# Performance work log

Hardware: AMD Instinct MI355X
Metric: run time of the kernel (lower is better)

Reference implementation:

```python
import jax, jax.numpy as jnp
import numpy as np

N = 20000
IN_C = 512
HID = 64
H1 = 8
OUT_C = 256
E = 320000
NEG_SLOPE = 0.2


def gat_conv(x, src, dst, W, a_src, a_dst, b, concat):
    # PyG GATConv (shared lin for src/dst), inference mode (no dropout).
    H, C = a_src.shape
    h = (x @ W).reshape(N, H, C)                      # [N,H,C]
    alpha_src = (h * a_src[None]).sum(-1)             # [N,H]
    alpha_dst = (h * a_dst[None]).sum(-1)             # [N,H]
    alpha = jax.nn.leaky_relu(alpha_src[src] + alpha_dst[dst], NEG_SLOPE)  # [E,H]
    # segment softmax over incoming edges of each dst node
    amax = jax.ops.segment_max(alpha, dst, num_segments=N)
    amax = jnp.where(jnp.isfinite(amax), amax, 0.0)
    ex = jnp.exp(alpha - amax[dst])
    denom = jax.ops.segment_sum(ex, dst, num_segments=N)
    coef = ex / (denom[dst] + 1e-16)                  # [E,H]
    msg = h[src] * coef[:, :, None]                   # [E,H,C]
    out = jax.ops.segment_sum(msg, dst, num_segments=N)  # [N,H,C]
    out = out.reshape(N, H * C) if concat else out.mean(axis=1)
    return out + b


def setup_inputs() -> dict:
    key = jax.random.key(0)
    ks = jax.random.split(key, 10)
    x = jax.random.normal(ks[0], (N, IN_C), dtype=jnp.float32)
    edge_index = jax.random.randint(ks[1], (2, E), 0, N, dtype=jnp.int32)
    s1 = 1.0 / np.sqrt(IN_C)
    s2 = 1.0 / np.sqrt(HID * H1)
    W1 = jax.random.uniform(ks[2], (IN_C, H1 * HID), jnp.float32, -s1, s1)
    att_src1 = jax.random.uniform(ks[3], (H1, HID), jnp.float32, -s1, s1)
    att_dst1 = jax.random.uniform(ks[4], (H1, HID), jnp.float32, -s1, s1)
    b1 = jnp.zeros((H1 * HID,), jnp.float32)
    W2 = jax.random.uniform(ks[5], (H1 * HID, OUT_C), jnp.float32, -s2, s2)
    att_src2 = jax.random.uniform(ks[6], (1, OUT_C), jnp.float32, -s2, s2)
    att_dst2 = jax.random.uniform(ks[7], (1, OUT_C), jnp.float32, -s2, s2)
    b2 = jnp.zeros((OUT_C,), jnp.float32)
    return {"x": x, "edge_index": edge_index, "W1": W1, "att_src1": att_src1,
            "att_dst1": att_dst1, "b1": b1, "W2": W2, "att_src2": att_src2,
            "att_dst2": att_dst2, "b2": b2}


def reference(x, edge_index, W1, att_src1, att_dst1, b1, W2, att_src2, att_dst2, b2):
    # add self-loops (PyG GATConv default add_self_loops=True)
    loop = jnp.arange(N, dtype=edge_index.dtype)
    src = jnp.concatenate([edge_index[0], loop])
    dst = jnp.concatenate([edge_index[1], loop])
    h = gat_conv(x, src, dst, W1, att_src1, att_dst1, b1, concat=True)
    h = jax.nn.elu(h)
    out = gat_conv(h, src, dst, W2, att_src2, att_dst2, b2, concat=False)
    return jax.nn.log_softmax(out, axis=1)
```

## Files before the change

### kernel.cpp

```cpp
#include <hip/hip_runtime.h>
#include <math.h>

#define N_NODES 20000
#define IN_CH   512
#define HID_TOT 512
#define OUT_CH  256
#define N_EDGE  320000
#define TOT_EDGE (N_EDGE + N_NODES)

typedef __attribute__((ext_vector_type(8))) short short8;
typedef __attribute__((ext_vector_type(4))) float f32x4;
typedef __attribute__((ext_vector_type(2))) float f32x2;

__device__ __forceinline__ ushort f2bf(float f) {
    union { float f; unsigned u; } v; v.f = f;
    unsigned u = v.u;
    return (ushort)((u + 0x7fffu + ((u >> 16) & 1u)) >> 16);
}

__device__ __forceinline__ void glds16(const ushort* g, ushort* l) {
    __builtin_amdgcn_global_load_lds(
        (const __attribute__((address_space(1))) void*)g,
        (__attribute__((address_space(3))) void*)l, 16, 0, 0);
}

__device__ __forceinline__ float lrelu(float a) { return fmaxf(a, 0.2f * a); }

#define NA_BLK (N_NODES * IN_CH / 4 / 256)
#define NB_BLK ((IN_CH / 64) * (HID_TOT / 4))
#define NC_BLK ((HID_TOT / 64) * (OUT_CH / 4))
#define NZ_BLK ((N_NODES + 255) / 256)
__global__ __launch_bounds__(256) void prep_kernel(const float* __restrict__ x,
                                                   ushort* __restrict__ xb,
                                                   const float* __restrict__ W1,
                                                   ushort* __restrict__ w1t,
                                                   const float* __restrict__ W2,
                                                   ushort* __restrict__ w2t,
                                                   int* __restrict__ counts,
                                                   float* __restrict__ as2,
                                                   float* __restrict__ ad2) {
    int b = blockIdx.x;
    int t = threadIdx.x;
    if (b < NA_BLK) {
        int i = b * 256 + t;
        float4 v = *(const float4*)&x[(size_t)i * 4];
        ushort4 o = make_ushort4(f2bf(v.x), f2bf(v.y), f2bf(v.z), f2bf(v.w));
        *(ushort4*)&xb[(size_t)i * 4] = o;
    } else if (b < NA_BLK + NB_BLK) {
        int bb = b - NA_BLK;
        int k = (bb & 7) * 64 + (t & 63);
        int n = (bb >> 3) * 4 + (t >> 6);
        w1t[(size_t)n * IN_CH + k] = f2bf(W1[(size_t)k * HID_TOT + n]);
    } else if (b < NA_BLK + NB_BLK + NC_BLK) {
        int bb = b - NA_BLK - NB_BLK;
        int k = (bb & 7) * 64 + (t & 63);
        int n = (bb >> 3) * 4 + (t >> 6);
        w2t[(size_t)n * HID_TOT + k] = f2bf(W2[(size_t)k * OUT_CH + n]);
    } else {
        int i = (b - NA_BLK - NB_BLK - NC_BLK) * 256 + t;
        if (i < N_NODES) { counts[i] = 0; as2[i] = 0.f; ad2[i] = 0.f; }
    }
}

__global__ void hist_kernel(const int* __restrict__ ei, int* __restrict__ counts) {
    int e = blockIdx.x * blockDim.x + threadIdx.x;
    if (e >= TOT_EDGE) return;
    int d = (e < N_EDGE) ? ei[N_EDGE + e] : (e - N_EDGE);
    atomicAdd(&counts[d], 1);
}

__global__ __launch_bounds__(1024) void scan_kernel(const int* __restrict__ counts,
                                                    int* __restrict__ offsets,
                                                    int* __restrict__ cursors) {
    const int C = (N_NODES + 1023) / 1024;
    int t = threadIdx.x;
    int lane = t & 63, wid = t >> 6;
    int base = t * C;
    int sum = 0;
#pragma unroll
    for (int i = 0; i < C; i++) {
        int idx = base + i;
        if (idx < N_NODES) sum += counts[idx];
    }
    int val = sum;
#pragma unroll
    for (int off = 1; off < 64; off <<= 1) {
        int y = __shfl_up(val, off);
        if (lane >= off) val += y;
    }
    __shared__ int wsum[16], woff[16], stotal;
    if (lane == 63) wsum[wid] = val;
    __syncthreads();
    if (t == 0) {
        int r = 0;
        for (int w = 0; w < 16; w++) { woff[w] = r; r += wsum[w]; }
        stotal = r;
    }
    __syncthreads();
    int running = woff[wid] + (val - sum);
#pragma unroll
    for (int i = 0; i < C; i++) {
        int idx = base + i;
        if (idx < N_NODES) {
            offsets[idx] = running;
            cursors[idx] = running;
            running += counts[idx];
        }
    }
    if (t == 0) offsets[N_NODES] = stotal;
}

__global__ void scatter_kernel(const int* __restrict__ ei, int* __restrict__ cursors,
                               int* __restrict__ srcs) {
    int e = blockIdx.x * blockDim.x + threadIdx.x;
    if (e >= TOT_EDGE) return;
    int s, d;
    if (e < N_EDGE) { s = ei[e]; d = ei[N_EDGE + e]; } else { s = e - N_EDGE; d = s; }
    int pos = atomicAdd(&cursors[d], 1);
    srcs[pos] = s;
}

__global__ __launch_bounds__(256, 2) void gemm_mfma_kernel(const ushort* __restrict__ A,
                                                           const ushort* __restrict__ Bt,
                                                           unsigned char* __restrict__ Cf8,
                                                           const float* __restrict__ asrc,
                                                           const float* __restrict__ adst,
                                                           float* __restrict__ as_out,
                                                           float* __restrict__ ad_out,
                                                           int M, int N, int K, int layer1) {
    __shared__ ushort As[128 * 64];
    __shared__ ushort Bs[128 * 64];
    int t = threadIdx.x;
    int lane = t & 63;
    int wave = t >> 6;
    int wr = (wave >> 1) * 64;
    int wc = (wave & 1) * 64;
    int bm = blockIdx.y * 128, bn = blockIdx.x * 128;
    int q = lane >> 4, l15 = lane & 15;

    const ushort* Aptr[4]; ushort* Alds[4];
    const ushort* Bptr[4]; ushort* Blds[4];
#pragma unroll
    for (int k = 0; k < 4; k++) {
        int c = t + 256 * k;
        int r = c >> 3, kqs = c & 7;
        int kqg = kqs ^ (r & 7);
        int ar = bm + r; if (ar >= M) ar = M - 1;
        Aptr[k] = A + (size_t)ar * K + kqg * 8;
        Alds[k] = &As[c * 8];
        Bptr[k] = Bt + (size_t)(bn + r) * K + kqg * 8;
        Blds[k] = &Bs[c * 8];
    }

    f32x4 acc[4][4];
#pragma unroll
    for (int i = 0; i < 4; i++)
#pragma unroll
        for (int j = 0; j < 4; j++) acc[i][j] = f32x4{0.f, 0.f, 0.f, 0.f};

    for (int k0 = 0; k0 < K; k0 += 64) {
        __syncthreads();
        glds16(Aptr[0] + k0, Alds[0]);
        glds16(Aptr[1] + k0, Alds[1]);
        glds16(Aptr[2] + k0, Alds[2]);
        glds16(Aptr[3] + k0, Alds[3]);
        glds16(Bptr[0] + k0, Blds[0]);
        glds16(Bptr[1] + k0, Blds[1]);
        glds16(Bptr[2] + k0, Blds[2]);
        glds16(Bptr[3] + k0, Blds[3]);
        __syncthreads();

#pragma unroll
        for (int s = 0; s < 2; s++) {
            int kq = s * 4 + q;
            short8 af[4], bf[4];
#pragma unroll
            for (int i = 0; i < 4; i++) {
                int row = wr + i * 16 + l15;
                int slot = kq ^ (row & 7);
                af[i] = *(const short8*)&As[row * 64 + slot * 8];
            }
#pragma unroll
            for (int j = 0; j < 4; j++) {
                int row = wc + j * 16 + l15;
                int slot = kq ^ (row & 7);
                bf[j] = *(const short8*)&Bs[row * 64 + slot * 8];
            }
#pragma unroll
            for (int i = 0; i < 4; i++)
#pragma unroll
                for (int j = 0; j < 4; j++)
                    acc[i][j] = __builtin_amdgcn_mfma_f32_16x16x32_bf16(af[i], bf[j], acc[i][j], 0, 0, 0);
        }
    }

    float av[4], dv[4];
#pragma unroll
    for (int j = 0; j < 4; j++) {
        int cg = bn + wc + j * 16 + l15;
        av[j] = asrc[cg];
        dv[j] = adst[cg];
    }
    float ps[4][4], pd[4][4];
#pragma unroll
    for (int i = 0; i < 4; i++)
#pragma unroll
        for (int r = 0; r < 4; r++) {
            float p = 0.f, d = 0.f;
#pragma unroll
            for (int j = 0; j < 4; j++) {
                p = fmaf(acc[i][j][r], av[j], p);
                d = fmaf(acc[i][j][r], dv[j], d);
            }
            ps[i][r] = p; pd[i][r] = d;
        }
#pragma unroll
    for (int off = 1; off < 16; off <<= 1) {
#pragma unroll
        for (int i = 0; i < 4; i++)
#pragma unroll
            for (int r = 0; r < 4; r++) {
                ps[i][r] += __shfl_xor(ps[i][r], off);
                pd[i][r] += __shfl_xor(pd[i][r], off);
            }
    }

    int hidx = blockIdx.x * 2 + (wave & 1);
#pragma unroll
    for (int i = 0; i < 4; i++) {
#pragma unroll
        for (int r = 0; r < 4; r++) {
            int rg = bm + wr + i * 16 + q * 4 + r;
            if (rg < M) {
#pragma unroll
                for (int j = 0; j < 4; j++) {
                    int cg = bn + wc + j * 16 + l15;
                    int w8 = __builtin_amdgcn_cvt_pk_fp8_f32(acc[i][j][r], acc[i][j][r], 0, false);
                    Cf8[(size_t)rg * N + cg] = (unsigned char)(w8 & 0xff);
                }
                if (l15 == 0) {
                    if (layer1) {
                        as_out[rg * 8 + hidx] = ps[i][r];
                        ad_out[rg * 8 + hidx] = pd[i][r];
                    } else {
                        atomicAdd(&as_out[rg], ps[i][r]);
                        atomicAdd(&ad_out[rg], pd[i][r]);
                    }
                }
            }
        }
    }
}

__global__ __launch_bounds__(256) void agg1_kernel(const unsigned char* __restrict__ h1f,
                                                   const float* __restrict__ as1,
                                                   const float* __restrict__ ad1,
                                                   const int* __restrict__ offsets,
                                                   const int* __restrict__ srcs,
                                                   const float* __restrict__ b1,
                                                   ushort* __restrict__ h1ab) {
    int v = blockIdx.x * 4 + (threadIdx.x >> 6);
    int lane = threadIdx.x & 63;
    int h = lane >> 3;
    int c8 = lane << 3;
    int s = offsets[v], e = offsets[v + 1];
    float adv = ad1[v * 8 + h];

    float denom = 0.f;
    float acc[8];
#pragma unroll
    for (int k = 0; k < 8; k++) acc[k] = 0.f;

    int i = s;
    for (; i + 8 <= e; i += 8) {
        int sn[8];
#pragma unroll
        for (int j = 0; j < 8; j++) sn[j] = srcs[i + j];
        uint2 r[8];
#pragma unroll
        for (int j = 0; j < 8; j++)
            r[j] = *(const uint2*)&h1f[(size_t)sn[j] * HID_TOT + c8];
        float w[8];
#pragma unroll
        for (int j = 0; j < 8; j++) {
            float a = lrelu(as1[sn[j] * 8 + h] + adv);
            w[j] = __expf(a);
            denom += w[j];
        }
#pragma unroll
        for (int j = 0; j < 8; j++) {
            f32x2 pa = __builtin_amdgcn_cvt_pk_f32_fp8(r[j].x, false);
            f32x2 pb = __builtin_amdgcn_cvt_pk_f32_fp8(r[j].x, true);
            f32x2 pc = __builtin_amdgcn_cvt_pk_f32_fp8(r[j].y, false);
            f32x2 pdd = __builtin_amdgcn_cvt_pk_f32_fp8(r[j].y, true);
            acc[0] = fmaf(w[j], pa.x, acc[0]); acc[1] = fmaf(w[j], pa.y, acc[1]);
            acc[2] = fmaf(w[j], pb.x, acc[2]); acc[3] = fmaf(w[j], pb.y, acc[3]);
            acc[4] = fmaf(w[j], pc.x, acc[4]); acc[5] = fmaf(w[j], pc.y, acc[5]);
            acc[6] = fmaf(w[j], pdd.x, acc[6]); acc[7] = fmaf(w[j], pdd.y, acc[7]);
        }
    }
    for (; i + 4 <= e; i += 4) {
        int sn[4];
#pragma unroll
        for (int j = 0; j < 4; j++) sn[j] = srcs[i + j];
        uint2 r[4];
#pragma unroll
        for (int j = 0; j < 4; j++)
            r[j] = *(const uint2*)&h1f[(size_t)sn[j] * HID_TOT + c8];
#pragma unroll
        for (int j = 0; j < 4; j++) {
            float a = lrelu(as1[sn[j] * 8 + h] + adv);
            float w = __expf(a);
            denom += w;
            f32x2 pa = __builtin_amdgcn_cvt_pk_f32_fp8(r[j].x, false);
            f32x2 pb = __builtin_amdgcn_cvt_pk_f32_fp8(r[j].x, true);
            f32x2 pc = __builtin_amdgcn_cvt_pk_f32_fp8(r[j].y, false);
            f32x2 pdd = __builtin_amdgcn_cvt_pk_f32_fp8(r[j].y, true);
            acc[0] = fmaf(w, pa.x, acc[0]); acc[1] = fmaf(w, pa.y, acc[1]);
            acc[2] = fmaf(w, pb.x, acc[2]); acc[3] = fmaf(w, pb.y, acc[3]);
            acc[4] = fmaf(w, pc.x, acc[4]); acc[5] = fmaf(w, pc.y, acc[5]);
            acc[6] = fmaf(w, pdd.x, acc[6]); acc[7] = fmaf(w, pdd.y, acc[7]);
        }
    }
    for (; i < e; i++) {
        int sn = srcs[i];
        uint2 r = *(const uint2*)&h1f[(size_t)sn * HID_TOT + c8];
        float a = lrelu(as1[sn * 8 + h] + adv);
        float w = __expf(a);
        denom += w;
        f32x2 pa = __builtin_amdgcn_cvt_pk_f32_fp8(r.x, false);
        f32x2 pb = __builtin_amdgcn_cvt_pk_f32_fp8(r.x, true);
        f32x2 pc = __builtin_amdgcn_cvt_pk_f32_fp8(r.y, false);
        f32x2 pdd = __builtin_amdgcn_cvt_pk_f32_fp8(r.y, true);
        acc[0] = fmaf(w, pa.x, acc[0]); acc[1] = fmaf(w, pa.y, acc[1]);
        acc[2] = fmaf(w, pb.x, acc[2]); acc[3] = fmaf(w, pb.y, acc[3]);
        acc[4] = fmaf(w, pc.x, acc[4]); acc[5] = fmaf(w, pc.y, acc[5]);
        acc[6] = fmaf(w, pdd.x, acc[6]); acc[7] = fmaf(w, pdd.y, acc[7]);
    }

    float inv = 1.f / (denom + 1e-16f);
    short8 ov;
#pragma unroll
    for (int k = 0; k < 8; k++) {
        float o = acc[k] * inv + b1[c8 + k];
        o = (o > 0.f) ? o : expm1f(o);
        ov[k] = (short)f2bf(o);
    }
    *(short8*)&h1ab[(size_t)v * HID_TOT + c8] = ov;
}

__global__ __launch_bounds__(256) void agg2_kernel(const unsigned char* __restrict__ h2f,
                                                   const float* __restrict__ as2,
                                                   const float* __restrict__ ad2,
                                                   const int* __restrict__ offsets,
                                                   const int* __restrict__ srcs,
                                                   const float* __restrict__ b2,
                                                   float* __restrict__ out) {
    int v = blockIdx.x * 4 + (threadIdx.x >> 6);
    int lane = threadIdx.x & 63;
    int c4 = lane << 2;
    int s = offsets[v], e = offsets[v + 1];
    float adv = ad2[v];

    float denom = 0.f;
    float acc[4];
#pragma unroll
    for (int k = 0; k < 4; k++) acc[k] = 0.f;

    int i = s;
    for (; i + 8 <= e; i += 8) {
        int sn[8];
#pragma unroll
        for (int j = 0; j < 8; j++) sn[j] = srcs[i + j];
        unsigned u[8];
#pragma unroll
        for (int j = 0; j < 8; j++)
            u[j] = *(const unsigned*)&h2f[(size_t)sn[j] * OUT_CH + c4];
        float w[8];
#pragma unroll
        for (int j = 0; j < 8; j++) {
            float a = lrelu(as2[sn[j]] + adv);
            w[j] = __expf(a);
            denom += w[j];
        }
#pragma unroll
        for (int j = 0; j < 8; j++) {
            f32x2 pa = __builtin_amdgcn_cvt_pk_f32_fp8(u[j], false);
            f32x2 pb = __builtin_amdgcn_cvt_pk_f32_fp8(u[j], true);
            acc[0] = fmaf(w[j], pa.x, acc[0]); acc[1] = fmaf(w[j], pa.y, acc[1]);
            acc[2] = fmaf(w[j], pb.x, acc[2]); acc[3] = fmaf(w[j], pb.y, acc[3]);
        }
    }
    for (; i + 4 <= e; i += 4) {
        int sn[4];
#pragma unroll
        for (int j = 0; j < 4; j++) sn[j] = srcs[i + j];
        unsigned u[4];
#pragma unroll
        for (int j = 0; j < 4; j++)
            u[j] = *(const unsigned*)&h2f[(size_t)sn[j] * OUT_CH + c4];
#pragma unroll
        for (int j = 0; j < 4; j++) {
            float a = lrelu(as2[sn[j]] + adv);
            float w = __expf(a);
            denom += w;
            f32x2 pa = __builtin_amdgcn_cvt_pk_f32_fp8(u[j], false);
            f32x2 pb = __builtin_amdgcn_cvt_pk_f32_fp8(u[j], true);
            acc[0] = fmaf(w, pa.x, acc[0]); acc[1] = fmaf(w, pa.y, acc[1]);
            acc[2] = fmaf(w, pb.x, acc[2]); acc[3] = fmaf(w, pb.y, acc[3]);
        }
    }
    for (; i < e; i++) {
        int sn = srcs[i];
        unsigned u = *(const unsigned*)&h2f[(size_t)sn * OUT_CH + c4];
        float a = lrelu(as2[sn] + adv);
        float w = __expf(a);
        denom += w;
        f32x2 pa = __builtin_amdgcn_cvt_pk_f32_fp8(u, false);
        f32x2 pb = __builtin_amdgcn_cvt_pk_f32_fp8(u, true);
        acc[0] = fmaf(w, pa.x, acc[0]); acc[1] = fmaf(w, pa.y, acc[1]);
        acc[2] = fmaf(w, pb.x, acc[2]); acc[3] = fmaf(w, pb.y, acc[3]);
    }

    float inv = 1.f / (denom + 1e-16f);
    float4 bb = *(const float4*)&b2[c4];
    float4 x;
    x.x = acc[0] * inv + bb.x; x.y = acc[1] * inv + bb.y;
    x.z = acc[2] * inv + bb.z; x.w = acc[3] * inv + bb.w;

    float mm = fmaxf(fmaxf(x.x, x.y), fmaxf(x.z, x.w));
#pragma unroll
    for (int off = 1; off < 64; off <<= 1) mm = fmaxf(mm, __shfl_xor(mm, off));
    float sum = __expf(x.x - mm) + __expf(x.y - mm) + __expf(x.z - mm) + __expf(x.w - mm);
#pragma unroll
    for (int off = 1; off < 64; off <<= 1) sum += __shfl_xor(sum, off);
    float ls = logf(sum);
    float4 o;
    o.x = x.x - mm - ls; o.y = x.y - mm - ls; o.z = x.z - mm - ls; o.w = x.w - mm - ls;
    *(float4*)&out[(size_t)v * OUT_CH + c4] = o;
}

static inline size_t align256(size_t x) { return (x + 255) & ~(size_t)255; }

extern "C" void kernel_launch(void* const* d_in, const int* in_sizes, int n_in,
                              void* d_out, int out_size, void* d_ws, size_t ws_size,
                              hipStream_t stream) {
    const float* x    = (const float*)d_in[0];
    const int*   ei   = (const int*)d_in[1];
    const float* W1   = (const float*)d_in[2];
    const float* as1w = (const float*)d_in[3];
    const float* ad1w = (const float*)d_in[4];
    const float* b1   = (const float*)d_in[5];
    const float* W2   = (const float*)d_in[6];
    const float* as2w = (const float*)d_in[7];
    const float* ad2w = (const float*)d_in[8];
    const float* b2   = (const float*)d_in[9];
    float* out = (float*)d_out;

    char* p = (char*)d_ws;
    unsigned char* h1f = (unsigned char*)p; p += align256((size_t)N_NODES * HID_TOT);
    unsigned char* h2f = (unsigned char*)p; p += align256((size_t)N_NODES * OUT_CH);
    ushort* xb   = (ushort*)p; p += align256(sizeof(ushort) * (size_t)N_NODES * IN_CH);
    ushort* h1ab = xb;
    ushort* w1t  = (ushort*)p; p += align256(sizeof(ushort) * (size_t)IN_CH * HID_TOT);
    ushort* w2t  = (ushort*)p; p += align256(sizeof(ushort) * (size_t)HID_TOT * OUT_CH);
    float* as1  = (float*)p; p += align256(sizeof(float) * (size_t)N_NODES * 8);
    float* ad1  = (float*)p; p += align256(sizeof(float) * (size_t)N_NODES * 8);
    float* as2  = (float*)p; p += align256(sizeof(float) * (size_t)N_NODES);
    float* ad2  = (float*)p; p += align256(sizeof(float) * (size_t)N_NODES);
    int* counts  = (int*)p; p += align256(sizeof(int) * (size_t)N_NODES);
    int* offsets = (int*)p; p += align256(sizeof(int) * (size_t)(N_NODES + 1));
    int* cursors = (int*)p; p += align256(sizeof(int) * (size_t)N_NODES);
    int* srcs    = (int*)p; p += align256(sizeof(int) * (size_t)TOT_EDGE);

    prep_kernel<<<NA_BLK + NB_BLK + NC_BLK + NZ_BLK, 256, 0, stream>>>(
        x, xb, W1, w1t, W2, w2t, counts, as2, ad2);

    int eb = (TOT_EDGE + 255) / 256;
    hist_kernel<<<eb, 256, 0, stream>>>(ei, counts);
    scan_kernel<<<1, 1024, 0, stream>>>(counts, offsets, cursors);
    scatter_kernel<<<eb, 256, 0, stream>>>(ei, cursors, srcs);

    gemm_mfma_kernel<<<dim3(HID_TOT / 128, (N_NODES + 127) / 128), 256, 0, stream>>>(
        xb, w1t, h1f, as1w, ad1w, as1, ad1, N_NODES, HID_TOT, IN_CH, 1);
    agg1_kernel<<<(N_NODES + 3) / 4, 256, 0, stream>>>(h1f, as1, ad1, offsets, srcs, b1, h1ab);

    gemm_mfma_kernel<<<dim3(OUT_CH / 128, (N_NODES + 127) / 128), 256, 0, stream>>>(
        h1ab, w2t, h2f, as2w, ad2w, as2, ad2, N_NODES, OUT_CH, HID_TOT, 0);
    agg2_kernel<<<(N_NODES + 3) / 4, 256, 0, stream>>>(h2f, as2, ad2, offsets, srcs, b2, out);
}
```

Baseline: 276.5 us.

## Split layer-1 aggregation per head and run layer-2 aggregation one wave per block

Layer-1 aggregation is remapped so each block handles a single attention head for 16 nodes. Sixteen lanes cover the head's 64 channels, four per lane, instead of one wave spanning all 512 channels of one node. The aim is to spread each node's gather over more independent waves and fewer registers, raising occupancy and latency hiding for the irregular neighbour reads. The cost is that each source row is fetched eight times in narrower 4-byte pieces, and the edge indices and source scores are read once per head. Layer-2 aggregation now launches 64-thread blocks, one node per block, instead of four nodes per 256-thread block.

New measurement: 275.6 us. No clear change (-0.3%).

```diff
diff --git a/kernel.cpp b/kernel.cpp
--- a/kernel.cpp
+++ b/kernel.cpp
@@ -259,106 +259,82 @@
                                                    const int* __restrict__ srcs,
                                                    const float* __restrict__ b1,
                                                    ushort* __restrict__ h1ab) {
-    int v = blockIdx.x * 4 + (threadIdx.x >> 6);
-    int lane = threadIdx.x & 63;
-    int h = lane >> 3;
-    int c8 = lane << 3;
+    int b = blockIdx.x;
+    int head = b & 7;
+    int grp = b >> 3;
+    int t = threadIdx.x;
+    int wave = t >> 6, lane = t & 63;
+    int qq = lane >> 4, l4 = lane & 15;
+    int v = grp * 16 + wave * 4 + qq;
+    int cofs = head * 64 + l4 * 4;
     int s = offsets[v], e = offsets[v + 1];
-    float adv = ad1[v * 8 + h];
+    float adv = ad1[v * 8 + head];
 
     float denom = 0.f;
-    float acc[8];
-#pragma unroll
-    for (int k = 0; k < 8; k++) acc[k] = 0.f;
+    float acc[4] = {0.f, 0.f, 0.f, 0.f};
 
     int i = s;
-    for (; i + 8 <= e; i += 8) {
-        int sn[8];
-#pragma unroll
-        for (int j = 0; j < 8; j++) sn[j] = srcs[i + j];
-        uint2 r[8];
-#pragma unroll
-        for (int j = 0; j < 8; j++)
-            r[j] = *(const uint2*)&h1f[(size_t)sn[j] * HID_TOT + c8];
-        float w[8];
-#pragma unroll
-        for (int j = 0; j < 8; j++) {
-            float a = lrelu(as1[sn[j] * 8 + h] + adv);
+    for (; i + 4 <= e; i += 4) {
+        int sn[4];
+#pragma unroll
+        for (int j = 0; j < 4; j++) sn[j] = srcs[i + j];
+        unsigned u[4];
+#pragma unroll
+        for (int j = 0; j < 4; j++)
+            u[j] = *(const unsigned*)&h1f[(size_t)sn[j] * HID_TOT + cofs];
+        float w[4];
+#pragma unroll
+        for (int j = 0; j < 4; j++) {
+            float a = lrelu(as1[sn[j] * 8 + head] + adv);
             w[j] = __expf(a);
             denom += w[j];
         }
 #pragma unroll
-        for (int j = 0; j < 8; j++) {
-            f32x2 pa = __builtin_amdgcn_cvt_pk_f32_fp8(r[j].x, false);
-            f32x2 pb = __builtin_amdgcn_cvt_pk_f32_fp8(r[j].x, true);
-            f32x2 pc = __builtin_amdgcn_cvt_pk_f32_fp8(r[j].y, false);
-            f32x2 pdd = __builtin_amdgcn_cvt_pk_f32_fp8(r[j].y, true);
+        for (int j = 0; j < 4; j++) {
+            f32x2 pa = __builtin_amdgcn_cvt_pk_f32_fp8(u[j], false);
+            f32x2 pb = __builtin_amdgcn_cvt_pk_f32_fp8(u[j], true);
             acc[0] = fmaf(w[j], pa.x, acc[0]); acc[1] = fmaf(w[j], pa.y, acc[1]);
             acc[2] = fmaf(w[j], pb.x, acc[2]); acc[3] = fmaf(w[j], pb.y, acc[3]);
-            acc[4] = fmaf(w[j], pc.x, acc[4]); acc[5] = fmaf(w[j], pc.y, acc[5]);
-            acc[6] = fmaf(w[j], pdd.x, acc[6]); acc[7] = fmaf(w[j], pdd.y, acc[7]);
-        }
-    }
-    for (; i + 4 <= e; i += 4) {
-        int sn[4];
-#pragma unroll
-        for (int j = 0; j < 4; j++) sn[j] = srcs[i + j];
-        uint2 r[4];
-#pragma unroll
-        for (int j = 0; j < 4; j++)
-            r[j] = *(const uint2*)&h1f[(size_t)sn[j] * HID_TOT + c8];
-#pragma unroll
-        for (int j = 0; j < 4; j++) {
-            float a = lrelu(as1[sn[j] * 8 + h] + adv);
-            float w = __expf(a);
-            denom += w;
-            f32x2 pa = __builtin_amdgcn_cvt_pk_f32_fp8(r[j].x, false);
-            f32x2 pb = __builtin_amdgcn_cvt_pk_f32_fp8(r[j].x, true);
-            f32x2 pc = __builtin_amdgcn_cvt_pk_f32_fp8(r[j].y, false);
-            f32x2 pdd = __builtin_amdgcn_cvt_pk_f32_fp8(r[j].y, true);
-            acc[0] = fmaf(w, pa.x, acc[0]); acc[1] = fmaf(w, pa.y, acc[1]);
-            acc[2] = fmaf(w, pb.x, acc[2]); acc[3] = fmaf(w, pb.y, acc[3]);
-            acc[4] = fmaf(w, pc.x, acc[4]); acc[5] = fmaf(w, pc.y, acc[5]);
-            acc[6] = fmaf(w, pdd.x, acc[6]); acc[7] = fmaf(w, pdd.y, acc[7]);
         }
     }
     for (; i < e; i++) {
         int sn = srcs[i];
-        uint2 r = *(const uint2*)&h1f[(size_t)sn * HID_TOT + c8];
-        float a = lrelu(as1[sn * 8 + h] + adv);
+        unsigned u = *(const unsigned*)&h1f[(size_t)sn * HID_TOT + cofs];
+        float a = lrelu(as1[sn * 8 + head] + adv);
         float w = __expf(a);
         denom += w;
-        f32x2 pa = __builtin_amdgcn_cvt_pk_f32_fp8(r.x, false);
-        f32x2 pb = __builtin_amdgcn_cvt_pk_f32_fp8(r.x, true);
-        f32x2 pc = __builtin_amdgcn_cvt_pk_f32_fp8(r.y, false);
-        f32x2 pdd = __builtin_amdgcn_cvt_pk_f32_fp8(r.y, true);
+        f32x2 pa = __builtin_amdgcn_cvt_pk_f32_fp8(u, false);
+        f32x2 pb = __builtin_amdgcn_cvt_pk_f32_fp8(u, true);
         acc[0] = fmaf(w, pa.x, acc[0]); acc[1] = fmaf(w, pa.y, acc[1]);
         acc[2] = fmaf(w, pb.x, acc[2]); acc[3] = fmaf(w, pb.y, acc[3]);
-        acc[4] = fmaf(w, pc.x, acc[4]); acc[5] = fmaf(w, pc.y, acc[5]);
-        acc[6] = fmaf(w, pdd.x, acc[6]); acc[7] = fmaf(w, pdd.y, acc[7]);
     }
 
     float inv = 1.f / (denom + 1e-16f);
-    short8 ov;
-#pragma unroll
-    for (int k = 0; k < 8; k++) {
-        float o = acc[k] * inv + b1[c8 + k];
-        o = (o > 0.f) ? o : expm1f(o);
-        ov[k] = (short)f2bf(o);
-    }
-    *(short8*)&h1ab[(size_t)v * HID_TOT + c8] = ov;
-}
-
-__global__ __launch_bounds__(256) void agg2_kernel(const unsigned char* __restrict__ h2f,
-                                                   const float* __restrict__ as2,
-                                                   const float* __restrict__ ad2,
-                                                   const int* __restrict__ offsets,
-                                                   const int* __restrict__ srcs,
-                                                   const float* __restrict__ b2,
-                                                   float* __restrict__ out) {
-    int v = blockIdx.x * 4 + (threadIdx.x >> 6);
-    int lane = threadIdx.x & 63;
-    int c4 = lane << 2;
+    ushort4 ov;
+    {
+        float o0 = acc[0] * inv + b1[cofs + 0];
+        float o1 = acc[1] * inv + b1[cofs + 1];
+        float o2 = acc[2] * inv + b1[cofs + 2];
+        float o3 = acc[3] * inv + b1[cofs + 3];
+        o0 = (o0 > 0.f) ? o0 : expm1f(o0);
+        o1 = (o1 > 0.f) ? o1 : expm1f(o1);
+        o2 = (o2 > 0.f) ? o2 : expm1f(o2);
+        o3 = (o3 > 0.f) ? o3 : expm1f(o3);
+        ov = make_ushort4(f2bf(o0), f2bf(o1), f2bf(o2), f2bf(o3));
+    }
+    *(ushort4*)&h1ab[(size_t)v * HID_TOT + cofs] = ov;
+}
+
+__global__ __launch_bounds__(64) void agg2_kernel(const unsigned char* __restrict__ h2f,
+                                                  const float* __restrict__ as2,
+                                                  const float* __restrict__ ad2,
+                                                  const int* __restrict__ offsets,
+                                                  const int* __restrict__ srcs,
+                                                  const float* __restrict__ b2,
+                                                  float* __restrict__ out) {
+    int v = blockIdx.x;
+    int t = threadIdx.x;
+    int c4 = t << 2;
     int s = offsets[v], e = offsets[v + 1];
     float adv = ad2[v];
 
@@ -483,9 +459,9 @@
 
     gemm_mfma_kernel<<<dim3(HID_TOT / 128, (N_NODES + 127) / 128), 256, 0, stream>>>(
         xb, w1t, h1f, as1w, ad1w, as1, ad1, N_NODES, HID_TOT, IN_CH, 1);
-    agg1_kernel<<<(N_NODES + 3) / 4, 256, 0, stream>>>(h1f, as1, ad1, offsets, srcs, b1, h1ab);
+    agg1_kernel<<<1250 * 8, 256, 0, stream>>>(h1f, as1, ad1, offsets, srcs, b1, h1ab);
 
     gemm_mfma_kernel<<<dim3(OUT_CH / 128, (N_NODES + 127) / 128), 256, 0, stream>>>(
         h1ab, w2t, h2f, as2w, ad2w, as2, ad2, N_NODES, OUT_CH, HID_TOT, 0);
-    agg2_kernel<<<(N_NODES + 3) / 4, 256, 0, stream>>>(h2f, as2, ad2, offsets, srcs, b2, out);
-}
+    agg2_kernel<<<N_NODES, 64, 0, stream>>>(h2f, as2, ad2, offsets, srcs, b2, out);
+}
```

## Remap aggregation kernels so each wave handles several nodes per head slice

Applied to the files above, without the earlier changes.

Layer-1 aggregation now gives each 64-lane block one head and 8 destination nodes, with 8 lanes per node reading 64 contiguous fp8 bytes. The attention-score arrays are stored head-major so those lanes read contiguous scores. Layer-2 aggregation handles two nodes per wave with 32 lanes each reading 8 bytes, and the log-softmax reduction shrinks to 32 lanes. The goal is to spread the gather latency of long edge lists across more independent nodes per wave. The trade-off is that different nodes in a wave have different degrees, causing divergence, and each source row of h1 is now fetched in eight separate head-sized pieces.

New measurement: 271.4 us. No clear change (-1.8%).

```diff
diff --git a/kernel.cpp b/kernel.cpp
--- a/kernel.cpp
+++ b/kernel.cpp
@@ -240,8 +240,8 @@
                 }
                 if (l15 == 0) {
                     if (layer1) {
-                        as_out[rg * 8 + hidx] = ps[i][r];
-                        ad_out[rg * 8 + hidx] = pd[i][r];
+                        as_out[hidx * N_NODES + rg] = ps[i][r];
+                        ad_out[hidx * N_NODES + rg] = pd[i][r];
                     } else {
                         atomicAdd(&as_out[rg], ps[i][r]);
                         atomicAdd(&ad_out[rg], pd[i][r]);
@@ -252,19 +252,25 @@
     }
 }
 
-__global__ __launch_bounds__(256) void agg1_kernel(const unsigned char* __restrict__ h1f,
-                                                   const float* __restrict__ as1,
-                                                   const float* __restrict__ ad1,
-                                                   const int* __restrict__ offsets,
-                                                   const int* __restrict__ srcs,
-                                                   const float* __restrict__ b1,
-                                                   ushort* __restrict__ h1ab) {
-    int v = blockIdx.x * 4 + (threadIdx.x >> 6);
-    int lane = threadIdx.x & 63;
-    int h = lane >> 3;
-    int c8 = lane << 3;
+__global__ __launch_bounds__(64) void agg1_kernel(const unsigned char* __restrict__ h1f,
+                                                  const float* __restrict__ as1,
+                                                  const float* __restrict__ ad1,
+                                                  const int* __restrict__ offsets,
+                                                  const int* __restrict__ srcs,
+                                                  const float* __restrict__ b1,
+                                                  ushort* __restrict__ h1ab) {
+    int b = blockIdx.x;
+    int head = b & 7;
+    int grp = b >> 3;
+    int lane = threadIdx.x;
+    int sub = lane >> 3;
+    int l8 = lane & 7;
+    int v = grp * 8 + sub;
+    int cofs = head * 64 + l8 * 8;
+    const unsigned char* hb = h1f + cofs;
+    const float* as1h = as1 + head * N_NODES;
     int s = offsets[v], e = offsets[v + 1];
-    float adv = ad1[v * 8 + h];
+    float adv = ad1[head * N_NODES + v];
 
     float denom = 0.f;
     float acc[8];
@@ -272,23 +278,23 @@
     for (int k = 0; k < 8; k++) acc[k] = 0.f;
 
     int i = s;
-    for (; i + 8 <= e; i += 8) {
-        int sn[8];
-#pragma unroll
-        for (int j = 0; j < 8; j++) sn[j] = srcs[i + j];
-        uint2 r[8];
-#pragma unroll
-        for (int j = 0; j < 8; j++)
-            r[j] = *(const uint2*)&h1f[(size_t)sn[j] * HID_TOT + c8];
-        float w[8];
-#pragma unroll
-        for (int j = 0; j < 8; j++) {
-            float a = lrelu(as1[sn[j] * 8 + h] + adv);
+    for (; i + 4 <= e; i += 4) {
+        int sn[4];
+#pragma unroll
+        for (int j = 0; j < 4; j++) sn[j] = srcs[i + j];
+        uint2 r[4];
+#pragma unroll
+        for (int j = 0; j < 4; j++)
+            r[j] = *(const uint2*)&hb[(size_t)sn[j] * HID_TOT];
+        float w[4];
+#pragma unroll
+        for (int j = 0; j < 4; j++) {
+            float a = lrelu(as1h[sn[j]] + adv);
             w[j] = __expf(a);
             denom += w[j];
         }
 #pragma unroll
-        for (int j = 0; j < 8; j++) {
+        for (int j = 0; j < 4; j++) {
             f32x2 pa = __builtin_amdgcn_cvt_pk_f32_fp8(r[j].x, false);
             f32x2 pb = __builtin_amdgcn_cvt_pk_f32_fp8(r[j].x, true);
             f32x2 pc = __builtin_amdgcn_cvt_pk_f32_fp8(r[j].y, false);
@@ -299,33 +305,10 @@
             acc[6] = fmaf(w[j], pdd.x, acc[6]); acc[7] = fmaf(w[j], pdd.y, acc[7]);
         }
     }
-    for (; i + 4 <= e; i += 4) {
-        int sn[4];
-#pragma unroll
-        for (int j = 0; j < 4; j++) sn[j] = srcs[i + j];
-        uint2 r[4];
-#pragma unroll
-        for (int j = 0; j < 4; j++)
-            r[j] = *(const uint2*)&h1f[(size_t)sn[j] * HID_TOT + c8];
-#pragma unroll
-        for (int j = 0; j < 4; j++) {
-            float a = lrelu(as1[sn[j] * 8 + h] + adv);
-            float w = __expf(a);
-            denom += w;
-            f32x2 pa = __builtin_amdgcn_cvt_pk_f32_fp8(r[j].x, false);
-            f32x2 pb = __builtin_amdgcn_cvt_pk_f32_fp8(r[j].x, true);
-            f32x2 pc = __builtin_amdgcn_cvt_pk_f32_fp8(r[j].y, false);
-            f32x2 pdd = __builtin_amdgcn_cvt_pk_f32_fp8(r[j].y, true);
-            acc[0] = fmaf(w, pa.x, acc[0]); acc[1] = fmaf(w, pa.y, acc[1]);
-            acc[2] = fmaf(w, pb.x, acc[2]); acc[3] = fmaf(w, pb.y, acc[3]);
-            acc[4] = fmaf(w, pc.x, acc[4]); acc[5] = fmaf(w, pc.y, acc[5]);
-            acc[6] = fmaf(w, pdd.x, acc[6]); acc[7] = fmaf(w, pdd.y, acc[7]);
-        }
-    }
     for (; i < e; i++) {
         int sn = srcs[i];
-        uint2 r = *(const uint2*)&h1f[(size_t)sn * HID_TOT + c8];
-        float a = lrelu(as1[sn * 8 + h] + adv);
+        uint2 r = *(const uint2*)&hb[(size_t)sn * HID_TOT];
+        float a = lrelu(as1h[sn] + adv);
         float w = __expf(a);
         denom += w;
         f32x2 pa = __builtin_amdgcn_cvt_pk_f32_fp8(r.x, false);
@@ -342,102 +325,101 @@
     short8 ov;
 #pragma unroll
     for (int k = 0; k < 8; k++) {
-        float o = acc[k] * inv + b1[c8 + k];
+        float o = acc[k] * inv + b1[cofs + k];
         o = (o > 0.f) ? o : expm1f(o);
         ov[k] = (short)f2bf(o);
     }
-    *(short8*)&h1ab[(size_t)v * HID_TOT + c8] = ov;
-}
-
-__global__ __launch_bounds__(256) void agg2_kernel(const unsigned char* __restrict__ h2f,
-                                                   const float* __restrict__ as2,
-                                                   const float* __restrict__ ad2,
-                                                   const int* __restrict__ offsets,
-                                                   const int* __restrict__ srcs,
-                                                   const float* __restrict__ b2,
-                                                   float* __restrict__ out) {
-    int v = blockIdx.x * 4 + (threadIdx.x >> 6);
-    int lane = threadIdx.x & 63;
-    int c4 = lane << 2;
+    *(short8*)&h1ab[(size_t)v * HID_TOT + cofs] = ov;
+}
+
+__global__ __launch_bounds__(64) void agg2_kernel(const unsigned char* __restrict__ h2f,
+                                                  const float* __restrict__ as2,
+                                                  const float* __restrict__ ad2,
+                                                  const int* __restrict__ offsets,
+                                                  const int* __restrict__ srcs,
+                                                  const float* __restrict__ b2,
+                                                  float* __restrict__ out) {
+    int lane = threadIdx.x;
+    int sub = lane >> 5;
+    int l32 = lane & 31;
+    int v = blockIdx.x * 2 + sub;
+    int c8 = l32 * 8;
+    const unsigned char* hb = h2f + c8;
     int s = offsets[v], e = offsets[v + 1];
     float adv = ad2[v];
 
     float denom = 0.f;
-    float acc[4];
-#pragma unroll
-    for (int k = 0; k < 4; k++) acc[k] = 0.f;
+    float acc[8];
+#pragma unroll
+    for (int k = 0; k < 8; k++) acc[k] = 0.f;
 
     int i = s;
-    for (; i + 8 <= e; i += 8) {
-        int sn[8];
-#pragma unroll
-        for (int j = 0; j < 8; j++) sn[j] = srcs[i + j];
-        unsigned u[8];
-#pragma unroll
-        for (int j = 0; j < 8; j++)
-            u[j] = *(const unsigned*)&h2f[(size_t)sn[j] * OUT_CH + c4];
-        float w[8];
-#pragma unroll
-        for (int j = 0; j < 8; j++) {
+    for (; i + 4 <= e; i += 4) {
+        int sn[4];
+#pragma unroll
+        for (int j = 0; j < 4; j++) sn[j] = srcs[i + j];
+        uint2 r[4];
+#pragma unroll
+        for (int j = 0; j < 4; j++)
+            r[j] = *(const uint2*)&hb[(size_t)sn[j] * OUT_CH];
+        float w[4];
+#pragma unroll
+        for (int j = 0; j < 4; j++) {
             float a = lrelu(as2[sn[j]] + adv);
             w[j] = __expf(a);
             denom += w[j];
         }
 #pragma unroll
-        for (int j = 0; j < 8; j++) {
-            f32x2 pa = __builtin_amdgcn_cvt_pk_f32_fp8(u[j], false);
-            f32x2 pb = __builtin_amdgcn_cvt_pk_f32_fp8(u[j], true);
+        for (int j = 0; j < 4; j++) {
+            f32x2 pa = __builtin_amdgcn_cvt_pk_f32_fp8(r[j].x, false);
+            f32x2 pb = __builtin_amdgcn_cvt_pk_f32_fp8(r[j].x, true);
+            f32x2 pc = __builtin_amdgcn_cvt_pk_f32_fp8(r[j].y, false);
+            f32x2 pdd = __builtin_amdgcn_cvt_pk_f32_fp8(r[j].y, true);
             acc[0] = fmaf(w[j], pa.x, acc[0]); acc[1] = fmaf(w[j], pa.y, acc[1]);
             acc[2] = fmaf(w[j], pb.x, acc[2]); acc[3] = fmaf(w[j], pb.y, acc[3]);
-        }
-    }
-    for (; i + 4 <= e; i += 4) {
-        int sn[4];
-#pragma unroll
-        for (int j = 0; j < 4; j++) sn[j] = srcs[i + j];
-        unsigned u[4];
-#pragma unroll
-        for (int j = 0; j < 4; j++)
-            u[j] = *(const unsigned*)&h2f[(size_t)sn[j] * OUT_CH + c4];
-#pragma unroll
-        for (int j = 0; j < 4; j++) {
-            float a = lrelu(as2[sn[j]] + adv);
-            float w = __expf(a);
-            denom += w;
-            f32x2 pa = __builtin_amdgcn_cvt_pk_f32_fp8(u[j], false);
-            f32x2 pb = __builtin_amdgcn_cvt_pk_f32_fp8(u[j], true);
-            acc[0] = fmaf(w, pa.x, acc[0]); acc[1] = fmaf(w, pa.y, acc[1]);
-            acc[2] = fmaf(w, pb.x, acc[2]); acc[3] = fmaf(w, pb.y, acc[3]);
+            acc[4] = fmaf(w[j], pc.x, acc[4]); acc[5] = fmaf(w[j], pc.y, acc[5]);
+            acc[6] = fmaf(w[j], pdd.x, acc[6]); acc[7] = fmaf(w[j], pdd.y, acc[7]);
         }
     }
     for (; i < e; i++) {
         int sn = srcs[i];
-        unsigned u = *(const unsigned*)&h2f[(size_t)sn * OUT_CH + c4];
+        uint2 r = *(const uint2*)&hb[(size_t)sn * OUT_CH];
         float a = lrelu(as2[sn] + adv);
         float w = __expf(a);
         denom += w;
-        f32x2 pa = __builtin_amdgcn_cvt_pk_f32_fp8(u, false);
-        f32x2 pb = __builtin_amdgcn_cvt_pk_f32_fp8(u, true);
+        f32x2 pa = __builtin_amdgcn_cvt_pk_f32_fp8(r.x, false);
+        f32x2 pb = __builtin_amdgcn_cvt_pk_f32_fp8(r.x, true);
+        f32x2 pc = __builtin_amdgcn_cvt_pk_f32_fp8(r.y, false);
+        f32x2 pdd = __builtin_amdgcn_cvt_pk_f32_fp8(r.y, true);
         acc[0] = fmaf(w, pa.x, acc[0]); acc[1] = fmaf(w, pa.y, acc[1]);
         acc[2] = fmaf(w, pb.x, acc[2]); acc[3] = fmaf(w, pb.y, acc[3]);
+        acc[4] = fmaf(w, pc.x, acc[4]); acc[5] = fmaf(w, pc.y, acc[5]);
+        acc[6] = fmaf(w, pdd.x, acc[6]); acc[7] = fmaf(w, pdd.y, acc[7]);
     }
 
     float inv = 1.f / (denom + 1e-16f);
-    float4 bb = *(const float4*)&b2[c4];
-    float4 x;
-    x.x = acc[0] * inv + bb.x; x.y = acc[1] * inv + bb.y;
-    x.z = acc[2] * inv + bb.z; x.w = acc[3] * inv + bb.w;
-
-    float mm = fmaxf(fmaxf(x.x, x.y), fmaxf(x.z, x.w));
-#pragma unroll
-    for (int off = 1; off < 64; off <<= 1) mm = fmaxf(mm, __shfl_xor(mm, off));
-    float sum = __expf(x.x - mm) + __expf(x.y - mm) + __expf(x.z - mm) + __expf(x.w - mm);
-#pragma unroll
-    for (int off = 1; off < 64; off <<= 1) sum += __shfl_xor(sum, off);
+    float xv[8];
+#pragma unroll
+    for (int k = 0; k < 8; k++) xv[k] = acc[k] * inv + b2[c8 + k];
+
+    float mm = xv[0];
+#pragma unroll
+    for (int k = 1; k < 8; k++) mm = fmaxf(mm, xv[k]);
+#pragma unroll
+    for (int off = 1; off < 32; off <<= 1) mm = fmaxf(mm, __shfl_xor(mm, off));
+    float sum = 0.f;
+#pragma unroll
+    for (int k = 0; k < 8; k++) sum += __expf(xv[k] - mm);
+#pragma unroll
+    for (int off = 1; off < 32; off <<= 1) sum += __shfl_xor(sum, off);
     float ls = logf(sum);
-    float4 o;
-    o.x = x.x - mm - ls; o.y = x.y - mm - ls; o.z = x.z - mm - ls; o.w = x.w - mm - ls;
-    *(float4*)&out[(size_t)v * OUT_CH + c4] = o;
+    float4 o0, o1;
+    o0.x = xv[0] - mm - ls; o0.y = xv[1] - mm - ls;
+    o0.z = xv[2] - mm - ls; o0.w = xv[3] - mm - ls;
+    o1.x = xv[4] - mm - ls; o1.y = xv[5] - mm - ls;
+    o1.z = xv[6] - mm - ls; o1.w = xv[7] - mm - ls;
+    *(float4*)&out[(size_t)v * OUT_CH + c8] = o0;
+    *(float4*)&out[(size_t)v * OUT_CH + c8 + 4] = o1;
 }
 
 static inline size_t align256(size_t x) { return (x + 255) & ~(size_t)255; }
@@ -483,9 +465,9 @@
 
     gemm_mfma_kernel<<<dim3(HID_TOT / 128, (N_NODES + 127) / 128), 256, 0, stream>>>(
         xb, w1t, h1f, as1w, ad1w, as1, ad1, N_NODES, HID_TOT, IN_CH, 1);
-    agg1_kernel<<<(N_NODES + 3) / 4, 256, 0, stream>>>(h1f, as1, ad1, offsets, srcs, b1, h1ab);
+    agg1_kernel<<<2500 * 8, 64, 0, stream>>>(h1f, as1, ad1, offsets, srcs, b1, h1ab);
 
     gemm_mfma_kernel<<<dim3(OUT_CH / 128, (N_NODES + 127) / 128), 256, 0, stream>>>(
         h1ab, w2t, h2f, as2w, ad2w, as2, ad2, N_NODES, OUT_CH, HID_TOT, 0);
-    agg2_kernel<<<(N_NODES + 3) / 4, 256, 0, stream>>>(h2f, as2, ad2, offsets, srcs, b2, out);
-}
+    agg2_kernel<<<N_NODES / 2, 64, 0, stream>>>(h2f, as2, ad2, offsets, srcs, b2, out);
+}
```
